# Optimization experiments

Hardware: AMD Instinct MI355X
Metric: run time of the kernel (lower is better)

Reference implementation:

```python
import jax, jax.numpy as jnp
import numpy as np

H, D = 16, 64  # num_attention_heads, attention_head_size
BASE = 10000.0

def _rope(q, k, seq_len):
    # RotaryPositionalEmbedding: inv_freq over arange(0, D, 2); emb = cat(freqs, freqs)
    inv_freq = 1.0 / (BASE ** (jnp.arange(0, D, 2, dtype=jnp.float32) / D))  # [D/2]=32
    pos = jnp.arange(seq_len, dtype=jnp.float32)
    freqs = jnp.outer(pos, inv_freq)            # [S, 32]; equals cos_emb[..., :d]
    cos, sin = jnp.cos(freqs), jnp.sin(freqs)   # [S, 32]
    d = D // 2                                   # 32: only first half of head dim rotated
    half = d // 2                                # 16: internal rotate-half within rot part
    def rot(x):  # x: [B, H, S, D]
        xr, xp = x[..., :d], x[..., d:]
        swapped = jnp.concatenate([xr[..., half:], xr[..., :half]], axis=-1)
        xr2 = xr * cos - swapped * sin
        return jnp.concatenate([xr2, xp], axis=-1)
    return rot(q), rot(k)

def setup_inputs() -> dict:
    key = jax.random.key(0)
    ks = jax.random.split(key, 9)
    B, S, E = 2, 2048, 1024
    std = 0.02  # initializer_range
    inp = {"hidden_states": jax.random.normal(ks[0], (B, S, E), jnp.float32)}
    for i, n in enumerate(["q", "k", "v", "d"]):
        inp[f"W{n}"] = jax.random.normal(ks[1 + 2 * i], (E, E), jnp.float32) * std
        inp[f"b{n}"] = jnp.zeros((E,), jnp.float32)
    return inp

def reference(hidden_states, Wq, bq, Wk, bk, Wv, bv, Wd, bd):
    B, S, E = hidden_states.shape
    def heads(x):  # [B,S,E] -> [B,H,S,D]
        return x.reshape(B, S, H, D).transpose(0, 2, 1, 3)
    q = heads(hidden_states @ Wq + bq)
    k = heads(hidden_states @ Wk + bk)
    v = heads(hidden_states @ Wv + bv)
    q, k = _rope(q, k, S)
    scores = jnp.einsum("bhqd,bhkd->bhqk", q, k) / jnp.sqrt(jnp.float32(D))
    causal = jnp.tril(jnp.ones((S, S), dtype=bool))
    scores = jnp.where(causal, scores, -jnp.inf)
    probs = jax.nn.softmax(scores, axis=-1)
    ctx = jnp.einsum("bhqk,bhkd->bhqd", probs, v)
    ctx = ctx.transpose(0, 2, 1, 3).reshape(B, S, E)
    return ctx @ Wd + bd
```

## Files before the change

### kernel.cpp

```cpp
#include <hip/hip_runtime.h>
#include <stdint.h>

typedef __bf16 bf8 __attribute__((ext_vector_type(8)));
typedef float f4 __attribute__((ext_vector_type(4)));
typedef float f16v __attribute__((ext_vector_type(16)));
typedef unsigned short us8 __attribute__((ext_vector_type(8)));
typedef unsigned short us4 __attribute__((ext_vector_type(4)));

#define MFMA16(a, b, c) __builtin_amdgcn_mfma_f32_16x16x32_bf16(a, b, c, 0, 0, 0)
#define MFMA32(a, b, c) __builtin_amdgcn_mfma_f32_32x32x16_bf16(a, b, c, 0, 0, 0)

__device__ __forceinline__ unsigned short f2b(float f) {
  union { float f; unsigned u; } x; x.f = f;
  unsigned u = x.u;
  u += 0x7fffu + ((u >> 16) & 1u);
  return (unsigned short)(u >> 16);
}

__device__ __forceinline__ unsigned pk2(float a, float b) {
  union { float f; unsigned u; } ua, ub; ua.f = a; ub.f = b;
  return __builtin_amdgcn_perm(ub.u + 0x8000u, ua.u + 0x8000u, 0x07060302u);
}

__device__ __forceinline__ void plswap(unsigned &a, unsigned &b) {
  asm("v_permlane32_swap_b32 %0, %1" : "+v"(a), "+v"(b));
}

__device__ __forceinline__ void gload16(const void* g, void* l) {
  __builtin_amdgcn_global_load_lds(
      (const __attribute__((address_space(1))) void*)g,
      (__attribute__((address_space(3))) void*)l, 16, 0, 0);
}

__global__ __launch_bounds__(256) void prep_kernel(
    const float* __restrict__ W0, const float* __restrict__ W1,
    const float* __restrict__ W2, const float* __restrict__ W3,
    unsigned short* __restrict__ T0, unsigned short* __restrict__ T1,
    unsigned short* __restrict__ T2, unsigned short* __restrict__ T3,
    const float* __restrict__ hid, unsigned short* __restrict__ hb) {
  if (blockIdx.z == 4) {
    int bi = blockIdx.x + 32 * blockIdx.y;
#pragma unroll
    for (int k = 0; k < 4; ++k) {
      int i = bi * 1024 + k * 256 + threadIdx.x;
      float4 v = ((const float4*)hid)[i];
      us4 r = { f2b(v.x), f2b(v.y), f2b(v.z), f2b(v.w) };
      *(us4*)(hb + (size_t)i * 4) = r;
    }
    return;
  }
  const float* W; unsigned short* Wt;
  if (blockIdx.z == 0)      { W = W0; Wt = T0; }
  else if (blockIdx.z == 1) { W = W1; Wt = T1; }
  else if (blockIdx.z == 2) { W = W2; Wt = T2; }
  else                      { W = W3; Wt = T3; }
  __shared__ float tile[32][33];
  int tx = threadIdx.x & 31, ty = threadIdx.x >> 5;
  int kb = blockIdx.x * 32, nb = blockIdx.y * 32;
#pragma unroll
  for (int j = 0; j < 32; j += 8)
    tile[ty + j][tx] = W[(size_t)(kb + ty + j) * 1024 + nb + tx];
  __syncthreads();
#pragma unroll
  for (int j = 0; j < 32; j += 8)
    Wt[(size_t)(nb + ty + j) * 1024 + kb + tx] = f2b(tile[tx][ty + j]);
}

__global__ __launch_bounds__(256) void gemm_qkv_kernel(
    const unsigned short* __restrict__ X,
    const unsigned short* __restrict__ Wqt, const unsigned short* __restrict__ Wkt,
    const unsigned short* __restrict__ Wvt,
    const float* __restrict__ bq, const float* __restrict__ bk,
    const float* __restrict__ bv,
    unsigned short* __restrict__ Qo, unsigned short* __restrict__ Ko,
    unsigned short* __restrict__ Vo) {
  const unsigned short* Wt; const float* bias; unsigned short* out;
  if (blockIdx.z == 0)      { Wt = Wqt; bias = bq; out = Qo; }
  else if (blockIdx.z == 1) { Wt = Wkt; bias = bk; out = Ko; }
  else                      { Wt = Wvt; bias = bv; out = Vo; }

  __shared__ unsigned short As[128 * 32];
  __shared__ unsigned short Bs[128 * 32];
  const int t = threadIdx.x;
  const int wave = t >> 6, lane = t & 63, quad = lane >> 4, l16 = lane & 15;
  const int wm = (wave >> 1) * 64, wn = (wave & 1) * 64;
  const int m0 = blockIdx.y * 128, n0 = blockIdx.x * 128;

  f4 acc[4][4];
#pragma unroll
  for (int mi = 0; mi < 4; ++mi)
#pragma unroll
    for (int ni = 0; ni < 4; ++ni) acc[mi][ni] = (f4)0.0f;

  for (int k0 = 0; k0 < 1024; k0 += 32) {
    __syncthreads();
#pragma unroll
    for (int it = 0; it < 2; ++it) {
      int chunk = it * 256 + wave * 64 + lane;
      int row = chunk >> 2, c = chunk & 3;
      gload16(&X[(size_t)(m0 + row) * 1024 + k0 + c * 8],
              &As[(size_t)(it * 256 + wave * 64) * 8]);
      gload16(&Wt[(size_t)(n0 + row) * 1024 + k0 + c * 8],
              &Bs[(size_t)(it * 256 + wave * 64) * 8]);
    }
    __syncthreads();
    bf8 a[4], b[4];
#pragma unroll
    for (int mi = 0; mi < 4; ++mi)
      a[mi] = *(const bf8*)&As[(wm + mi * 16 + l16) * 32 + quad * 8];
#pragma unroll
    for (int ni = 0; ni < 4; ++ni)
      b[ni] = *(const bf8*)&Bs[(wn + ni * 16 + l16) * 32 + quad * 8];
#pragma unroll
    for (int mi = 0; mi < 4; ++mi)
#pragma unroll
      for (int ni = 0; ni < 4; ++ni)
        acc[mi][ni] = MFMA16(a[mi], b[ni], acc[mi][ni]);
  }

  float biasv[4];
#pragma unroll
  for (int ni = 0; ni < 4; ++ni) biasv[ni] = bias[n0 + wn + ni * 16 + l16];

  if (blockIdx.z < 2) {
    const float kr = 13.287712379549449f / 32.0f;
    const float f0 = exp2f(-(float)l16 * kr);
    const float f1 = exp2f(-(float)(l16 + 16) * kr);
    const float qs = (blockIdx.z == 0) ? 0.18033688011112042f : 1.0f;
#pragma unroll
    for (int mi = 0; mi < 4; ++mi) {
#pragma unroll
      for (int r = 0; r < 4; ++r) {
        int m = m0 + wm + mi * 16 + quad * 4 + r;
        float s = (float)(m & 2047);
        float s0, c0, s1, c1;
        __sincosf(s * f0, &s0, &c0);
        __sincosf(s * f1, &s1, &c1);
        float v0 = acc[mi][0][r] + biasv[0];
        float v1 = acc[mi][1][r] + biasv[1];
        acc[mi][0][r] = (v0 * c0 - v1 * s0) * qs;
        acc[mi][1][r] = (v1 * c1 - v0 * s1) * qs;
        acc[mi][2][r] = (acc[mi][2][r] + biasv[2]) * qs;
        acc[mi][3][r] = (acc[mi][3][r] + biasv[3]) * qs;
      }
    }
    if (blockIdx.z == 0) {
#pragma unroll
      for (int ni = 0; ni < 4; ++ni) {
        int n = n0 + wn + ni * 16 + l16;
        int h = n >> 6, d = n & 63;
#pragma unroll
        for (int mi = 0; mi < 4; ++mi) {
#pragma unroll
          for (int r = 0; r < 4; ++r) {
            int m = m0 + wm + mi * 16 + quad * 4 + r;
            int b_ = m >> 11, s = m & 2047;
            out[(size_t)(((b_ << 4) | h) * 2048 + s) * 64 + d] = f2b(acc[mi][ni][r]);
          }
        }
      }
    } else {
#pragma unroll
      for (int ni = 0; ni < 4; ++ni) {
        int n = n0 + wn + ni * 16 + l16;
        int h = n >> 6, d = n & 63;
        int cpart = (d >> 4) * 512 + ((d >> 3) & 1) * 256 + (d & 7);
#pragma unroll
        for (int mi = 0; mi < 4; ++mi) {
#pragma unroll
          for (int r = 0; r < 4; ++r) {
            int m = m0 + wm + mi * 16 + quad * 4 + r;
            int b_ = m >> 11, s = m & 2047;
            size_t off = (size_t)((b_ << 4) | h) * 131072
                       + (size_t)(s >> 5) * 2048 + (s & 31) * 8 + cpart;
            out[off] = f2b(acc[mi][ni][r]);
          }
        }
      }
    }
  } else {
#pragma unroll
    for (int ni = 0; ni < 4; ++ni) {
      int n = n0 + wn + ni * 16 + l16;
      int h = n >> 6, d = n & 63;
      int dpart = ((d >> 5) & 1) * 2048 + (d & 31) * 8;
#pragma unroll
      for (int mi = 0; mi < 4; ++mi) {
        int m = m0 + wm + mi * 16 + quad * 4;
        int b_ = m >> 11, s = m & 2047;
        us4 w = { f2b(acc[mi][ni][0] + biasv[ni]), f2b(acc[mi][ni][1] + biasv[ni]),
                  f2b(acc[mi][ni][2] + biasv[ni]), f2b(acc[mi][ni][3] + biasv[ni]) };
        size_t off = (size_t)((b_ << 4) | h) * 131072
                   + (size_t)(s >> 6) * 4096 + ((s >> 4) & 3) * 512
                   + ((s >> 3) & 1) * 256 + dpart + (s & 7);
        *(us4*)&out[off] = w;
      }
    }
  }
}

__global__ __launch_bounds__(256) void flash_attn_kernel(
    const unsigned short* __restrict__ Q, const unsigned short* __restrict__ K,
    const unsigned short* __restrict__ Vt, unsigned short* __restrict__ ctx) {
  __shared__ __align__(16) float osh[2][64][36];
  __shared__ float lsh[2][64];
  const int t = threadIdx.x;
  const int lane = t & 63;
  const int wave = t >> 6, l32 = lane & 31, hl = lane >> 5;
  const int sub = wave >> 1;
  const int kh  = wave & 1;

  const int id = blockIdx.x;
  const int bh = id & 31;
  const int j = id >> 5;
  const int qt = (j & 16) ? (31 - (j & 15)) : (j & 15);
  const int b = bh >> 4, h = bh & 15;

  const unsigned short* Qh = Q + (size_t)bh * 131072;
  const unsigned short* Kh = K + (size_t)bh * 131072;
  const unsigned short* Vh = Vt + (size_t)bh * 131072;

  const int wrow0 = qt * 64 + sub * 32;
  const int q = wrow0 + l32;

  bf8 qb[4];
#pragma unroll
  for (int c = 0; c < 4; ++c)
    qb[c] = *(const bf8*)&Qh[(size_t)q * 64 + c * 16 + hl * 8];

  f16v o0 = (f16v)0.0f, o1 = (f16v)0.0f;
  float sum = 0.0f;

  bf8 kfA[2][4], kfB[2][4], vf[2][4];
  const int nk = qt + 1;
  const int kb = kh ? (nk >> 1) : 0;
  const int ke = kh ? nk : (nk >> 1);

  auto loadK = [&](bf8 (&kf)[2][4], int kt) {
    const unsigned short* p = Kh + (size_t)kt * 4096 + lane * 8;
#pragma unroll
    for (int mt = 0; mt < 2; ++mt)
#pragma unroll
      for (int c = 0; c < 4; ++c)
        kf[mt][c] = *(const bf8*)&p[mt * 2048 + c * 512];
  };

  auto step = [&](int kt, bf8 (&kf)[2][4]) {
    const int k0 = kt * 64;
    const unsigned short* pv = Vh + (size_t)kt * 4096 + lane * 8;
#pragma unroll
    for (int dt = 0; dt < 2; ++dt)
#pragma unroll
      for (int c = 0; c < 4; ++c)
        vf[dt][c] = *(const bf8*)&pv[dt * 2048 + c * 512];

    f16v s0 = (f16v)0.0f, s1 = (f16v)0.0f;
#pragma unroll
    for (int c = 0; c < 4; ++c) {
      s0 = MFMA32(kf[0][c], qb[c], s0);
      s1 = MFMA32(kf[1][c], qb[c], s1);
    }
    if (kt == nk - 1) {
#pragma unroll
      for (int gg = 0; gg < 4; ++gg)
#pragma unroll
        for (int i = 0; i < 4; ++i) {
          int kk = k0 + gg * 8 + hl * 4 + i;
          if (kk > q) s0[gg * 4 + i] = -3e38f;
          if (kk + 32 > q) s1[gg * 4 + i] = -3e38f;
        }
    }
    uint2 pd2[8];
#pragma unroll
    for (int gg = 0; gg < 4; ++gg) {
      float p0 = exp2f(s0[gg * 4 + 0]), p1 = exp2f(s0[gg * 4 + 1]);
      float p2 = exp2f(s0[gg * 4 + 2]), p3 = exp2f(s0[gg * 4 + 3]);
      sum += (p0 + p1) + (p2 + p3);
      pd2[gg].x = pk2(p0, p1); pd2[gg].y = pk2(p2, p3);
      float r0 = exp2f(s1[gg * 4 + 0]), r1 = exp2f(s1[gg * 4 + 1]);
      float r2 = exp2f(s1[gg * 4 + 2]), r3 = exp2f(s1[gg * 4 + 3]);
      sum += (r0 + r1) + (r2 + r3);
      pd2[4 + gg].x = pk2(r0, r1); pd2[4 + gg].y = pk2(r2, r3);
    }
    uint4 fr[4];
#pragma unroll
    for (int c = 0; c < 4; ++c) {
      unsigned ax = pd2[2 * c].x, bx = pd2[2 * c + 1].x;
      unsigned ay = pd2[2 * c].y, by = pd2[2 * c + 1].y;
      plswap(ax, bx);
      plswap(ay, by);
      fr[c].x = ax; fr[c].y = ay; fr[c].z = bx; fr[c].w = by;
    }
#pragma unroll
    for (int c = 0; c < 4; ++c) {
      union { uint4 u; bf8 v; } pv2; pv2.u = fr[c];
      o0 = MFMA32(vf[0][c], pv2.v, o0);
      o1 = MFMA32(vf[1][c], pv2.v, o1);
    }
  };

  if (kb < ke) {
    loadK(kfA, kb);
    int kt = kb;
    while (true) {
      if (kt + 1 < ke) loadK(kfB, kt + 1);
      step(kt, kfA);
      ++kt; if (kt >= ke) break;
      if (kt + 1 < ke) loadK(kfA, kt + 1);
      step(kt, kfB);
      ++kt; if (kt >= ke) break;
    }
  }

  float lpart = sum + __shfl_xor(sum, 32);

  if (kh == 0) {
#pragma unroll
    for (int gg = 0; gg < 4; ++gg) {
      f4 w0 = { o0[gg * 4 + 0], o0[gg * 4 + 1], o0[gg * 4 + 2], o0[gg * 4 + 3] };
      *(f4*)&osh[sub][lane][gg * 4] = w0;
      f4 w1 = { o1[gg * 4 + 0], o1[gg * 4 + 1], o1[gg * 4 + 2], o1[gg * 4 + 3] };
      *(f4*)&osh[sub][lane][16 + gg * 4] = w1;
    }
    lsh[sub][lane] = lpart;
  }
  __syncthreads();
  if (kh == 1) {
    float inv = 1.0f / (lpart + lsh[sub][lane]);
#pragma unroll
    for (int gg = 0; gg < 4; ++gg) {
      int d0 = gg * 8 + hl * 4;
      f4 a0 = *(f4*)&osh[sub][lane][gg * 4];
      f4 a1 = *(f4*)&osh[sub][lane][16 + gg * 4];
      us4 w0 = { f2b((o0[gg * 4 + 0] + a0[0]) * inv), f2b((o0[gg * 4 + 1] + a0[1]) * inv),
                 f2b((o0[gg * 4 + 2] + a0[2]) * inv), f2b((o0[gg * 4 + 3] + a0[3]) * inv) };
      *(us4*)&ctx[((size_t)(b * 2048 + q)) * 1024 + h * 64 + d0] = w0;
      us4 w1 = { f2b((o1[gg * 4 + 0] + a1[0]) * inv), f2b((o1[gg * 4 + 1] + a1[1]) * inv),
                 f2b((o1[gg * 4 + 2] + a1[2]) * inv), f2b((o1[gg * 4 + 3] + a1[3]) * inv) };
      *(us4*)&ctx[((size_t)(b * 2048 + q)) * 1024 + h * 64 + 32 + d0] = w1;
    }
  }
}

__global__ __launch_bounds__(256) void gemm_out_kernel(
    const unsigned short* __restrict__ A,
    const unsigned short* __restrict__ Wt,
    const float* __restrict__ bias, float* __restrict__ out) {
  __shared__ unsigned short As[64 * 32];
  __shared__ unsigned short Bs[128 * 32];
  const int t = threadIdx.x;
  const int wave = t >> 6, lane = t & 63, quad = lane >> 4, l16 = lane & 15;
  const int wm = (wave & 1) * 32, wn = (wave >> 1) * 64;
  const int m0 = blockIdx.y * 64, n0 = blockIdx.x * 128;

  f4 acc[2][4];
#pragma unroll
  for (int mi = 0; mi < 2; ++mi)
#pragma unroll
    for (int ni = 0; ni < 4; ++ni) acc[mi][ni] = (f4)0.0f;

  for (int k0 = 0; k0 < 1024; k0 += 32) {
    __syncthreads();
    {
      int chunk = wave * 64 + lane;
      int row = chunk >> 2, c = chunk & 3;
      gload16(&A[(size_t)(m0 + row) * 1024 + k0 + c * 8],
              &As[(size_t)(wave * 64) * 8]);
#pragma unroll
      for (int it = 0; it < 2; ++it) {
        int ch = it * 256 + wave * 64 + lane;
        int rw = ch >> 2, cc = ch & 3;
        gload16(&Wt[(size_t)(n0 + rw) * 1024 + k0 + cc * 8],
                &Bs[(size_t)(it * 256 + wave * 64) * 8]);
      }
    }
    __syncthreads();
    bf8 a[2], b[4];
#pragma unroll
    for (int mi = 0; mi < 2; ++mi)
      a[mi] = *(const bf8*)&As[(wm + mi * 16 + l16) * 32 + quad * 8];
#pragma unroll
    for (int ni = 0; ni < 4; ++ni)
      b[ni] = *(const bf8*)&Bs[(wn + ni * 16 + l16) * 32 + quad * 8];
#pragma unroll
    for (int mi = 0; mi < 2; ++mi)
#pragma unroll
      for (int ni = 0; ni < 4; ++ni)
        acc[mi][ni] = MFMA16(a[mi], b[ni], acc[mi][ni]);
  }
#pragma unroll
  for (int ni = 0; ni < 4; ++ni) {
    int n = n0 + wn + ni * 16 + l16;
    float bv_ = bias[n];
#pragma unroll
    for (int mi = 0; mi < 2; ++mi) {
#pragma unroll
      for (int r = 0; r < 4; ++r) {
        int m = m0 + wm + mi * 16 + quad * 4 + r;
        out[(size_t)m * 1024 + n] = acc[mi][ni][r] + bv_;
      }
    }
  }
}

extern "C" void kernel_launch(void* const* d_in, const int* in_sizes, int n_in,
                              void* d_out, int out_size, void* d_ws, size_t ws_size,
                              hipStream_t stream) {
  const float* hidden = (const float*)d_in[0];
  const float* Wq = (const float*)d_in[1];
  const float* bq = (const float*)d_in[2];
  const float* Wk = (const float*)d_in[3];
  const float* bk = (const float*)d_in[4];
  const float* Wv = (const float*)d_in[5];
  const float* bv = (const float*)d_in[6];
  const float* Wd = (const float*)d_in[7];
  const float* bd = (const float*)d_in[8];
  float* out = (float*)d_out;

  char* ws = (char*)d_ws;
  unsigned short* Xb  = (unsigned short*)(ws);
  unsigned short* Wqt = (unsigned short*)(ws + ( 8ull << 20));
  unsigned short* Wkt = (unsigned short*)(ws + (10ull << 20));
  unsigned short* Wvt = (unsigned short*)(ws + (12ull << 20));
  unsigned short* Wdt = (unsigned short*)(ws + (14ull << 20));
  unsigned short* Qb  = (unsigned short*)(ws + (16ull << 20));
  unsigned short* Kb  = (unsigned short*)(ws + (24ull << 20));
  unsigned short* Vb  = (unsigned short*)(ws + (32ull << 20));
  unsigned short* Cb  = (unsigned short*)(ws + (40ull << 20));

  prep_kernel<<<dim3(32, 32, 5), 256, 0, stream>>>(
      Wq, Wk, Wv, Wd, Wqt, Wkt, Wvt, Wdt, hidden, Xb);
  gemm_qkv_kernel<<<dim3(8, 32, 3), 256, 0, stream>>>(
      Xb, Wqt, Wkt, Wvt, bq, bk, bv, Qb, Kb, Vb);
  flash_attn_kernel<<<1024, 256, 0, stream>>>(Qb, Kb, Vb, Cb);
  gemm_out_kernel<<<dim3(8, 64), 256, 0, stream>>>(Cb, Wdt, bd, out);
}
```

Baseline: 205.3 us.

## Double-buffer V tiles with K, use hardware bf16 pack, add MFMA priority

V fragments are now prefetched one tile ahead together with K in a double-buffered register pipeline, so the PV MFMAs no longer wait on V loads issued in the same step. The manual round-and-perm bf16 packing is replaced with the v_cvt_pk_bf16_f32 instruction. s_setprio raises wave priority around the MFMA blocks to help interleave math across waves. Double-buffering V doubles its register footprint, which could lower occupancy or cause spills.

```diff
diff --git a/kernel.cpp b/kernel.cpp
--- a/kernel.cpp
+++ b/kernel.cpp
@@ -17,9 +17,10 @@
   return (unsigned short)(u >> 16);
 }
 
-__device__ __forceinline__ unsigned pk2(float a, float b) {
-  union { float f; unsigned u; } ua, ub; ua.f = a; ub.f = b;
-  return __builtin_amdgcn_perm(ub.u + 0x8000u, ua.u + 0x8000u, 0x07060302u);
+__device__ __forceinline__ unsigned cvtpk(float a, float b) {
+  unsigned r;
+  asm("v_cvt_pk_bf16_f32 %0, %1, %2" : "=v"(r) : "v"(a), "v"(b));
+  return r;
 }
 
 __device__ __forceinline__ void plswap(unsigned &a, unsigned &b) {
@@ -231,35 +232,33 @@
   f16v o0 = (f16v)0.0f, o1 = (f16v)0.0f;
   float sum = 0.0f;
 
-  bf8 kfA[2][4], kfB[2][4], vf[2][4];
+  bf8 kfA[2][4], kfB[2][4], vfA[2][4], vfB[2][4];
   const int nk = qt + 1;
   const int kb = kh ? (nk >> 1) : 0;
   const int ke = kh ? nk : (nk >> 1);
 
-  auto loadK = [&](bf8 (&kf)[2][4], int kt) {
+  auto loadKV = [&](bf8 (&kf)[2][4], bf8 (&vf)[2][4], int kt) {
     const unsigned short* p = Kh + (size_t)kt * 4096 + lane * 8;
+    const unsigned short* pv = Vh + (size_t)kt * 4096 + lane * 8;
 #pragma unroll
     for (int mt = 0; mt < 2; ++mt)
 #pragma unroll
-      for (int c = 0; c < 4; ++c)
+      for (int c = 0; c < 4; ++c) {
         kf[mt][c] = *(const bf8*)&p[mt * 2048 + c * 512];
+        vf[mt][c] = *(const bf8*)&pv[mt * 2048 + c * 512];
+      }
   };
 
-  auto step = [&](int kt, bf8 (&kf)[2][4]) {
+  auto step = [&](int kt, bf8 (&kf)[2][4], bf8 (&vf)[2][4]) {
     const int k0 = kt * 64;
-    const unsigned short* pv = Vh + (size_t)kt * 4096 + lane * 8;
-#pragma unroll
-    for (int dt = 0; dt < 2; ++dt)
-#pragma unroll
-      for (int c = 0; c < 4; ++c)
-        vf[dt][c] = *(const bf8*)&pv[dt * 2048 + c * 512];
-
     f16v s0 = (f16v)0.0f, s1 = (f16v)0.0f;
+    __builtin_amdgcn_s_setprio(1);
 #pragma unroll
     for (int c = 0; c < 4; ++c) {
       s0 = MFMA32(kf[0][c], qb[c], s0);
       s1 = MFMA32(kf[1][c], qb[c], s1);
     }
+    __builtin_amdgcn_s_setprio(0);
     if (kt == nk - 1) {
 #pragma unroll
       for (int gg = 0; gg < 4; ++gg)
@@ -276,11 +275,11 @@
       float p0 = exp2f(s0[gg * 4 + 0]), p1 = exp2f(s0[gg * 4 + 1]);
       float p2 = exp2f(s0[gg * 4 + 2]), p3 = exp2f(s0[gg * 4 + 3]);
       sum += (p0 + p1) + (p2 + p3);
-      pd2[gg].x = pk2(p0, p1); pd2[gg].y = pk2(p2, p3);
+      pd2[gg].x = cvtpk(p0, p1); pd2[gg].y = cvtpk(p2, p3);
       float r0 = exp2f(s1[gg * 4 + 0]), r1 = exp2f(s1[gg * 4 + 1]);
       float r2 = exp2f(s1[gg * 4 + 2]), r3 = exp2f(s1[gg * 4 + 3]);
       sum += (r0 + r1) + (r2 + r3);
-      pd2[4 + gg].x = pk2(r0, r1); pd2[4 + gg].y = pk2(r2, r3);
+      pd2[4 + gg].x = cvtpk(r0, r1); pd2[4 + gg].y = cvtpk(r2, r3);
     }
     uint4 fr[4];
 #pragma unroll
@@ -291,23 +290,25 @@
       plswap(ay, by);
       fr[c].x = ax; fr[c].y = ay; fr[c].z = bx; fr[c].w = by;
     }
+    __builtin_amdgcn_s_setprio(1);
 #pragma unroll
     for (int c = 0; c < 4; ++c) {
       union { uint4 u; bf8 v; } pv2; pv2.u = fr[c];
       o0 = MFMA32(vf[0][c], pv2.v, o0);
       o1 = MFMA32(vf[1][c], pv2.v, o1);
     }
+    __builtin_amdgcn_s_setprio(0);
   };
 
   if (kb < ke) {
-    loadK(kfA, kb);
+    loadKV(kfA, vfA, kb);
     int kt = kb;
     while (true) {
-      if (kt + 1 < ke) loadK(kfB, kt + 1);
-      step(kt, kfA);
+      if (kt + 1 < ke) loadKV(kfB, vfB, kt + 1);
+      step(kt, kfA, vfA);
       ++kt; if (kt >= ke) break;
-      if (kt + 1 < ke) loadK(kfA, kt + 1);
-      step(kt, kfB);
+      if (kt + 1 < ke) loadKV(kfA, vfA, kt + 1);
+      step(kt, kfB, vfB);
       ++kt; if (kt >= ke) break;
     }
   }
```

After: 207.0 us. Within noise of the previous version (+0.8%).

## Split attention into 32-row tiles with 4-way KV split and setprio

Applied to the files above, without the earlier changes.

Each attention block now handles one 32-row query tile, with all four waves splitting the key range into quarters, and the grid doubles to 2048 blocks ordered longest tile first. The partial outputs and row sums from three waves are reduced through shared memory by wave 0. MFMA sections are wrapped in s_setprio to favour matrix issue, and the manual bf16 packing is replaced with the hardware v_cvt_pk_bf16_f32 instruction. The aim is better load balance and occupancy across the causal triangle, at the cost of more reduction traffic and less K/V reuse per block.

```diff
diff --git a/kernel.cpp b/kernel.cpp
--- a/kernel.cpp
+++ b/kernel.cpp
@@ -17,9 +17,10 @@
   return (unsigned short)(u >> 16);
 }
 
-__device__ __forceinline__ unsigned pk2(float a, float b) {
-  union { float f; unsigned u; } ua, ub; ua.f = a; ub.f = b;
-  return __builtin_amdgcn_perm(ub.u + 0x8000u, ua.u + 0x8000u, 0x07060302u);
+__device__ __forceinline__ unsigned cvtpk(float a, float b) {
+  unsigned r;
+  asm("v_cvt_pk_bf16_f32 %0, %1, %2" : "=v"(r) : "v"(a), "v"(b));
+  return r;
 }
 
 __device__ __forceinline__ void plswap(unsigned &a, unsigned &b) {
@@ -202,26 +203,22 @@
 __global__ __launch_bounds__(256) void flash_attn_kernel(
     const unsigned short* __restrict__ Q, const unsigned short* __restrict__ K,
     const unsigned short* __restrict__ Vt, unsigned short* __restrict__ ctx) {
-  __shared__ __align__(16) float osh[2][64][36];
-  __shared__ float lsh[2][64];
+  __shared__ __align__(16) float osh[3][64][36];
+  __shared__ float lsh[3][64];
   const int t = threadIdx.x;
   const int lane = t & 63;
   const int wave = t >> 6, l32 = lane & 31, hl = lane >> 5;
-  const int sub = wave >> 1;
-  const int kh  = wave & 1;
 
   const int id = blockIdx.x;
   const int bh = id & 31;
-  const int j = id >> 5;
-  const int qt = (j & 16) ? (31 - (j & 15)) : (j & 15);
+  const int tile = 63 - (id >> 5);
   const int b = bh >> 4, h = bh & 15;
 
   const unsigned short* Qh = Q + (size_t)bh * 131072;
   const unsigned short* Kh = K + (size_t)bh * 131072;
   const unsigned short* Vh = Vt + (size_t)bh * 131072;
 
-  const int wrow0 = qt * 64 + sub * 32;
-  const int q = wrow0 + l32;
+  const int q = tile * 32 + l32;
 
   bf8 qb[4];
 #pragma unroll
@@ -232,9 +229,10 @@
   float sum = 0.0f;
 
   bf8 kfA[2][4], kfB[2][4], vf[2][4];
-  const int nk = qt + 1;
-  const int kb = kh ? (nk >> 1) : 0;
-  const int ke = kh ? nk : (nk >> 1);
+  const int nk = (tile >> 1) + 1;
+  const int nq = (nk + 3) >> 2;
+  const int kb = wave * nq;
+  const int ke = (kb + nq < nk) ? (kb + nq) : nk;
 
   auto loadK = [&](bf8 (&kf)[2][4], int kt) {
     const unsigned short* p = Kh + (size_t)kt * 4096 + lane * 8;
@@ -255,11 +253,13 @@
         vf[dt][c] = *(const bf8*)&pv[dt * 2048 + c * 512];
 
     f16v s0 = (f16v)0.0f, s1 = (f16v)0.0f;
+    __builtin_amdgcn_s_setprio(1);
 #pragma unroll
     for (int c = 0; c < 4; ++c) {
       s0 = MFMA32(kf[0][c], qb[c], s0);
       s1 = MFMA32(kf[1][c], qb[c], s1);
     }
+    __builtin_amdgcn_s_setprio(0);
     if (kt == nk - 1) {
 #pragma unroll
       for (int gg = 0; gg < 4; ++gg)
@@ -276,11 +276,11 @@
       float p0 = exp2f(s0[gg * 4 + 0]), p1 = exp2f(s0[gg * 4 + 1]);
       float p2 = exp2f(s0[gg * 4 + 2]), p3 = exp2f(s0[gg * 4 + 3]);
       sum += (p0 + p1) + (p2 + p3);
-      pd2[gg].x = pk2(p0, p1); pd2[gg].y = pk2(p2, p3);
+      pd2[gg].x = cvtpk(p0, p1); pd2[gg].y = cvtpk(p2, p3);
       float r0 = exp2f(s1[gg * 4 + 0]), r1 = exp2f(s1[gg * 4 + 1]);
       float r2 = exp2f(s1[gg * 4 + 2]), r3 = exp2f(s1[gg * 4 + 3]);
       sum += (r0 + r1) + (r2 + r3);
-      pd2[4 + gg].x = pk2(r0, r1); pd2[4 + gg].y = pk2(r2, r3);
+      pd2[4 + gg].x = cvtpk(r0, r1); pd2[4 + gg].y = cvtpk(r2, r3);
     }
     uint4 fr[4];
 #pragma unroll
@@ -291,12 +291,14 @@
       plswap(ay, by);
       fr[c].x = ax; fr[c].y = ay; fr[c].z = bx; fr[c].w = by;
     }
+    __builtin_amdgcn_s_setprio(1);
 #pragma unroll
     for (int c = 0; c < 4; ++c) {
       union { uint4 u; bf8 v; } pv2; pv2.u = fr[c];
       o0 = MFMA32(vf[0][c], pv2.v, o0);
       o1 = MFMA32(vf[1][c], pv2.v, o1);
     }
+    __builtin_amdgcn_s_setprio(0);
   };
 
   if (kb < ke) {
@@ -314,29 +316,37 @@
 
   float lpart = sum + __shfl_xor(sum, 32);
 
-  if (kh == 0) {
+  if (wave) {
 #pragma unroll
     for (int gg = 0; gg < 4; ++gg) {
       f4 w0 = { o0[gg * 4 + 0], o0[gg * 4 + 1], o0[gg * 4 + 2], o0[gg * 4 + 3] };
-      *(f4*)&osh[sub][lane][gg * 4] = w0;
+      *(f4*)&osh[wave - 1][lane][gg * 4] = w0;
       f4 w1 = { o1[gg * 4 + 0], o1[gg * 4 + 1], o1[gg * 4 + 2], o1[gg * 4 + 3] };
-      *(f4*)&osh[sub][lane][16 + gg * 4] = w1;
-    }
-    lsh[sub][lane] = lpart;
+      *(f4*)&osh[wave - 1][lane][16 + gg * 4] = w1;
+    }
+    lsh[wave - 1][lane] = lpart;
   }
   __syncthreads();
-  if (kh == 1) {
-    float inv = 1.0f / (lpart + lsh[sub][lane]);
+  if (wave == 0) {
+    float inv = 1.0f / (lpart + lsh[0][lane] + lsh[1][lane] + lsh[2][lane]);
 #pragma unroll
     for (int gg = 0; gg < 4; ++gg) {
       int d0 = gg * 8 + hl * 4;
-      f4 a0 = *(f4*)&osh[sub][lane][gg * 4];
-      f4 a1 = *(f4*)&osh[sub][lane][16 + gg * 4];
-      us4 w0 = { f2b((o0[gg * 4 + 0] + a0[0]) * inv), f2b((o0[gg * 4 + 1] + a0[1]) * inv),
-                 f2b((o0[gg * 4 + 2] + a0[2]) * inv), f2b((o0[gg * 4 + 3] + a0[3]) * inv) };
+      f4 a0 = *(f4*)&osh[0][lane][gg * 4];
+      f4 b0 = *(f4*)&osh[1][lane][gg * 4];
+      f4 c0 = *(f4*)&osh[2][lane][gg * 4];
+      f4 a1 = *(f4*)&osh[0][lane][16 + gg * 4];
+      f4 b1 = *(f4*)&osh[1][lane][16 + gg * 4];
+      f4 c1 = *(f4*)&osh[2][lane][16 + gg * 4];
+      us4 w0 = { f2b((o0[gg * 4 + 0] + a0[0] + b0[0] + c0[0]) * inv),
+                 f2b((o0[gg * 4 + 1] + a0[1] + b0[1] + c0[1]) * inv),
+                 f2b((o0[gg * 4 + 2] + a0[2] + b0[2] + c0[2]) * inv),
+                 f2b((o0[gg * 4 + 3] + a0[3] + b0[3] + c0[3]) * inv) };
       *(us4*)&ctx[((size_t)(b * 2048 + q)) * 1024 + h * 64 + d0] = w0;
-      us4 w1 = { f2b((o1[gg * 4 + 0] + a1[0]) * inv), f2b((o1[gg * 4 + 1] + a1[1]) * inv),
-                 f2b((o1[gg * 4 + 2] + a1[2]) * inv), f2b((o1[gg * 4 + 3] + a1[3]) * inv) };
+      us4 w1 = { f2b((o1[gg * 4 + 0] + a1[0] + b1[0] + c1[0]) * inv),
+                 f2b((o1[gg * 4 + 1] + a1[1] + b1[1] + c1[1]) * inv),
+                 f2b((o1[gg * 4 + 2] + a1[2] + b1[2] + c1[2]) * inv),
+                 f2b((o1[gg * 4 + 3] + a1[3] + b1[3] + c1[3]) * inv) };
       *(us4*)&ctx[((size_t)(b * 2048 + q)) * 1024 + h * 64 + 32 + d0] = w1;
     }
   }
@@ -432,6 +442,6 @@
       Wq, Wk, Wv, Wd, Wqt, Wkt, Wvt, Wdt, hidden, Xb);
   gemm_qkv_kernel<<<dim3(8, 32, 3), 256, 0, stream>>>(
       Xb, Wqt, Wkt, Wvt, bq, bk, bv, Qb, Kb, Vb);
-  flash_attn_kernel<<<1024, 256, 0, stream>>>(Qb, Kb, Vb, Cb);
+  flash_attn_kernel<<<2048, 256, 0, stream>>>(Qb, Kb, Vb, Cb);
   gemm_out_kernel<<<dim3(8, 64), 256, 0, stream>>>(Cb, Wdt, bd, out);
 }
```

Measured after the change: 215.2 us. +4.8%, slower.

## Double GEMM K-tile to 64 with XOR-swizzled LDS layout

Applied to the files above, without the earlier changes.

Both the QKV projection and output projection GEMMs now stage 64-wide K slices per iteration instead of 32, halving the number of barrier-separated load/compute rounds. The LDS tiles use an XOR swizzle on 16-byte chunks (chunk index xor row&7) applied at global-load time and undone on the MFMA fragment reads, to avoid bank conflicts from the wider 128-byte row stride. This doubles shared memory per block, which may reduce occupancy.

```diff
diff --git a/kernel.cpp b/kernel.cpp
--- a/kernel.cpp
+++ b/kernel.cpp
@@ -79,8 +79,8 @@
   else if (blockIdx.z == 1) { Wt = Wkt; bias = bk; out = Ko; }
   else                      { Wt = Wvt; bias = bv; out = Vo; }
 
-  __shared__ unsigned short As[128 * 32];
-  __shared__ unsigned short Bs[128 * 32];
+  __shared__ unsigned short As[128 * 64];
+  __shared__ unsigned short Bs[128 * 64];
   const int t = threadIdx.x;
   const int wave = t >> 6, lane = t & 63, quad = lane >> 4, l16 = lane & 15;
   const int wm = (wave >> 1) * 64, wn = (wave & 1) * 64;
@@ -92,30 +92,35 @@
 #pragma unroll
     for (int ni = 0; ni < 4; ++ni) acc[mi][ni] = (f4)0.0f;
 
-  for (int k0 = 0; k0 < 1024; k0 += 32) {
+  for (int k0 = 0; k0 < 1024; k0 += 64) {
     __syncthreads();
 #pragma unroll
-    for (int it = 0; it < 2; ++it) {
+    for (int it = 0; it < 4; ++it) {
       int chunk = it * 256 + wave * 64 + lane;
-      int row = chunk >> 2, c = chunk & 3;
-      gload16(&X[(size_t)(m0 + row) * 1024 + k0 + c * 8],
+      int row = chunk >> 3, cc = chunk & 7;
+      int csw = cc ^ (row & 7);
+      gload16(&X[(size_t)(m0 + row) * 1024 + k0 + csw * 8],
               &As[(size_t)(it * 256 + wave * 64) * 8]);
-      gload16(&Wt[(size_t)(n0 + row) * 1024 + k0 + c * 8],
+      gload16(&Wt[(size_t)(n0 + row) * 1024 + k0 + csw * 8],
               &Bs[(size_t)(it * 256 + wave * 64) * 8]);
     }
     __syncthreads();
-    bf8 a[4], b[4];
-#pragma unroll
-    for (int mi = 0; mi < 4; ++mi)
-      a[mi] = *(const bf8*)&As[(wm + mi * 16 + l16) * 32 + quad * 8];
-#pragma unroll
-    for (int ni = 0; ni < 4; ++ni)
-      b[ni] = *(const bf8*)&Bs[(wn + ni * 16 + l16) * 32 + quad * 8];
-#pragma unroll
-    for (int mi = 0; mi < 4; ++mi)
+#pragma unroll
+    for (int kk = 0; kk < 2; ++kk) {
+      const int sw = (kk * 4 + quad) ^ (l16 & 7);
+      bf8 a[4], b[4];
+#pragma unroll
+      for (int mi = 0; mi < 4; ++mi)
+        a[mi] = *(const bf8*)&As[(wm + mi * 16 + l16) * 64 + sw * 8];
 #pragma unroll
       for (int ni = 0; ni < 4; ++ni)
-        acc[mi][ni] = MFMA16(a[mi], b[ni], acc[mi][ni]);
+        b[ni] = *(const bf8*)&Bs[(wn + ni * 16 + l16) * 64 + sw * 8];
+#pragma unroll
+      for (int mi = 0; mi < 4; ++mi)
+#pragma unroll
+        for (int ni = 0; ni < 4; ++ni)
+          acc[mi][ni] = MFMA16(a[mi], b[ni], acc[mi][ni]);
+    }
   }
 
   float biasv[4];
@@ -346,8 +351,8 @@
     const unsigned short* __restrict__ A,
     const unsigned short* __restrict__ Wt,
     const float* __restrict__ bias, float* __restrict__ out) {
-  __shared__ unsigned short As[64 * 32];
-  __shared__ unsigned short Bs[128 * 32];
+  __shared__ unsigned short As[64 * 64];
+  __shared__ unsigned short Bs[128 * 64];
   const int t = threadIdx.x;
   const int wave = t >> 6, lane = t & 63, quad = lane >> 4, l16 = lane & 15;
   const int wm = (wave & 1) * 32, wn = (wave >> 1) * 64;
@@ -359,34 +364,41 @@
 #pragma unroll
     for (int ni = 0; ni < 4; ++ni) acc[mi][ni] = (f4)0.0f;
 
-  for (int k0 = 0; k0 < 1024; k0 += 32) {
+  for (int k0 = 0; k0 < 1024; k0 += 64) {
     __syncthreads();
     {
-      int chunk = wave * 64 + lane;
-      int row = chunk >> 2, c = chunk & 3;
-      gload16(&A[(size_t)(m0 + row) * 1024 + k0 + c * 8],
-              &As[(size_t)(wave * 64) * 8]);
 #pragma unroll
       for (int it = 0; it < 2; ++it) {
-        int ch = it * 256 + wave * 64 + lane;
-        int rw = ch >> 2, cc = ch & 3;
-        gload16(&Wt[(size_t)(n0 + rw) * 1024 + k0 + cc * 8],
+        int chunk = it * 256 + wave * 64 + lane;
+        int row = chunk >> 3, cc = chunk & 7;
+        gload16(&A[(size_t)(m0 + row) * 1024 + k0 + (cc ^ (row & 7)) * 8],
+                &As[(size_t)(it * 256 + wave * 64) * 8]);
+      }
+#pragma unroll
+      for (int it = 0; it < 4; ++it) {
+        int chunk = it * 256 + wave * 64 + lane;
+        int row = chunk >> 3, cc = chunk & 7;
+        gload16(&Wt[(size_t)(n0 + row) * 1024 + k0 + (cc ^ (row & 7)) * 8],
                 &Bs[(size_t)(it * 256 + wave * 64) * 8]);
       }
     }
     __syncthreads();
-    bf8 a[2], b[4];
-#pragma unroll
-    for (int mi = 0; mi < 2; ++mi)
-      a[mi] = *(const bf8*)&As[(wm + mi * 16 + l16) * 32 + quad * 8];
-#pragma unroll
-    for (int ni = 0; ni < 4; ++ni)
-      b[ni] = *(const bf8*)&Bs[(wn + ni * 16 + l16) * 32 + quad * 8];
-#pragma unroll
-    for (int mi = 0; mi < 2; ++mi)
+#pragma unroll
+    for (int kk = 0; kk < 2; ++kk) {
+      const int sw = (kk * 4 + quad) ^ (l16 & 7);
+      bf8 a[2], b[4];
+#pragma unroll
+      for (int mi = 0; mi < 2; ++mi)
+        a[mi] = *(const bf8*)&As[(wm + mi * 16 + l16) * 64 + sw * 8];
 #pragma unroll
       for (int ni = 0; ni < 4; ++ni)
-        acc[mi][ni] = MFMA16(a[mi], b[ni], acc[mi][ni]);
+        b[ni] = *(const bf8*)&Bs[(wn + ni * 16 + l16) * 64 + sw * 8];
+#pragma unroll
+      for (int mi = 0; mi < 2; ++mi)
+#pragma unroll
+        for (int ni = 0; ni < 4; ++ni)
+          acc[mi][ni] = MFMA16(a[mi], b[ni], acc[mi][ni]);
+    }
   }
 #pragma unroll
   for (int ni = 0; ni < 4; ++ni) {
```

New measurement: 199.1 us. 3.0% less time.
